# Optimization experiments

Measured on AMD Instinct MI355X. Metric: run time of the kernel, lower is better.

Reference implementation:

```python
import jax, jax.numpy as jnp
import numpy as np

N_NODES = 10000
N_EDGES = 320000
N_PAIRS = 1000000
IN_C = 256
HID_C = 256
LAT_C = 128


def _linear_init(key, fan_in, fan_out, bias=True):
    k1, k2 = jax.random.split(key)
    bound = 1.0 / np.sqrt(fan_in)
    W = jax.random.uniform(k1, (fan_in, fan_out), minval=-bound, maxval=bound, dtype=jnp.float32)
    if bias:
        b = jax.random.uniform(k2, (fan_out,), minval=-bound, maxval=bound, dtype=jnp.float32)
        return W, b
    return W


def setup_inputs() -> dict:
    key = jax.random.key(0)
    ks = jax.random.split(key, 12)
    x = jax.random.normal(ks[0], (N_NODES, IN_C), dtype=jnp.float32)
    edge_index = jax.random.randint(ks[1], (2, N_EDGES), 0, N_NODES, dtype=jnp.int32)
    edge_weight_norm = jax.random.uniform(ks[2], (N_EDGES,), dtype=jnp.float32)
    edge_list = jax.random.randint(ks[3], (2, N_PAIRS), 0, N_NODES, dtype=jnp.int32)
    # GraphConv layer params: lin_rel (bias) on aggregated msgs, lin_root (no bias) on self
    W_rel1, b_rel1 = _linear_init(ks[4], IN_C, HID_C)
    W_root1 = _linear_init(ks[5], IN_C, HID_C, bias=False)
    W_rel2, b_rel2 = _linear_init(ks[6], HID_C, LAT_C)
    W_root2 = _linear_init(ks[7], HID_C, LAT_C, bias=False)
    W_rel3, b_rel3 = _linear_init(ks[8], LAT_C, LAT_C)
    W_root3 = _linear_init(ks[9], LAT_C, LAT_C, bias=False)
    # decoder MLP: Linear(2*LAT, HID) -> ReLU -> Linear(HID, 1)
    Wd1, bd1 = _linear_init(ks[10], 2 * LAT_C, HID_C)
    Wd2, bd2 = _linear_init(ks[11], HID_C, 1)
    return {
        'x': x, 'edge_index': edge_index, 'edge_weight_norm': edge_weight_norm,
        'edge_list': edge_list,
        'W_rel1': W_rel1, 'b_rel1': b_rel1, 'W_root1': W_root1,
        'W_rel2': W_rel2, 'b_rel2': b_rel2, 'W_root2': W_root2,
        'W_rel3': W_rel3, 'b_rel3': b_rel3, 'W_root3': W_root3,
        'Wd1': Wd1, 'bd1': bd1, 'Wd2': Wd2, 'bd2': bd2,
    }


def _graph_conv(h, src, dst, ew, W_rel, b_rel, W_root):
    # message: edge-weighted source features, sum-aggregated at destination
    msg = ew[:, None] * h[src]                        # [E, C_in]
    agg = jax.ops.segment_sum(msg, dst, num_segments=N_NODES)  # [N, C_in]
    return agg @ W_rel + b_rel + h @ W_root           # [N, C_out]


def reference(x, edge_index, edge_weight_norm, edge_list,
              W_rel1, b_rel1, W_root1,
              W_rel2, b_rel2, W_root2,
              W_rel3, b_rel3, W_root3,
              Wd1, bd1, Wd2, bd2):
    src, dst = edge_index[0], edge_index[1]
    h = jax.nn.relu(_graph_conv(x, src, dst, edge_weight_norm, W_rel1, b_rel1, W_root1))
    h = jax.nn.relu(_graph_conv(h, src, dst, edge_weight_norm, W_rel2, b_rel2, W_root2))
    z = _graph_conv(h, src, dst, edge_weight_norm, W_rel3, b_rel3, W_root3)  # [N, LAT]
    # decode edge list: gather pairs, concat, MLP
    h_cat = jnp.concatenate([z[edge_list[0]], z[edge_list[1]]], axis=1)  # [P, 2*LAT]
    hid = jax.nn.relu(h_cat @ Wd1 + bd1)
    out = (hid @ Wd2 + bd2).squeeze(-1)               # [P]
    return out
```

## Files before the change

kernel.cpp:

```cpp
#include <hip/hip_runtime.h>

#define N_NODES 10000
#define N_EDGES 320000
#define N_PAIRS 1000000
#define NBUCK 8
#define DBW 1250
#define SBW 1250
#define PSB 512
#define SLOTB 84
#define GXM 157

typedef unsigned short ushort_t;
typedef __attribute__((ext_vector_type(8))) short short8;
typedef __attribute__((ext_vector_type(4))) float floatx4;
typedef _Float16 half2_t __attribute__((ext_vector_type(2)));

__device__ inline float blo(unsigned int u) { return __uint_as_float(u << 16); }
__device__ inline float bhi(unsigned int u) { return __uint_as_float(u & 0xffff0000u); }
__device__ inline ushort_t f2bf(float f) {
    unsigned int u = __float_as_uint(f);
    unsigned int r = (u + 0x7fffu + ((u >> 16) & 1u)) >> 16;
    return (ushort_t)r;
}
__device__ inline float bf2f(ushort_t b) { return __uint_as_float(((unsigned int)b) << 16); }
__device__ inline void stout(float* p, float v) { *p = v; }
__device__ inline void stout(ushort_t* p, float v) { *p = f2bf(v); }
__device__ inline void stout(_Float16* p, float v) { *p = (_Float16)v; }


__device__ void dev_pstage(int bid, const int* __restrict__ el,
                           int2* __restrict__ stage, int* __restrict__ scnt) {
    __shared__ int lcur[64];
    int t = threadIdx.x;
    if (t < 64) lcur[t] = 0;
    __syncthreads();
    const int STR = PSB * 256;
    int i0 = bid * 256 + t;
#pragma unroll
    for (int k = 0; k < 8; k++) {
        int i = i0 + k * STR;
        if (i < N_PAIRS) {
            int s = el[i], d = el[N_PAIRS + i];
            int c = (d / DBW) * 8 + s / SBW;
            int r = atomicAdd(&lcur[c], 1);
            stage[((size_t)c * PSB + bid) * SLOTB + r] = make_int2(s | (d << 14), i);
        }
    }
    __syncthreads();
    if (t < 64) {
        int n = lcur[t];
        scnt[t * PSB + bid] = n;
        int np = (n + 7) & ~7;
        int2* sp = stage + ((size_t)t * PSB + bid) * SLOTB;
        for (int i = n; i < np; ++i) sp[i] = make_int2(-1, -1);
    }
}

__device__ void dev_hist(int bid, const int* __restrict__ ei, int* __restrict__ cnt) {
    int e = bid * 256 + threadIdx.x;
    if (e < N_EDGES) atomicAdd(&cnt[ei[N_EDGES + e]], 1);
}

__device__ void dev_xsplit(int bid, const float* __restrict__ x, ushort_t* __restrict__ xh) {
    int i = bid * 256 + threadIdx.x;
    if (i >= N_NODES * 256 / 4) return;
    float4 f = ((const float4*)x)[i];
    union { uint2 v; ushort_t u[4]; } H;
    H.u[0] = f2bf(f.x); H.u[1] = f2bf(f.y); H.u[2] = f2bf(f.z); H.u[3] = f2bf(f.w);
    ((uint2*)xh)[i] = H.v;
}

__device__ void dev_wsplit(int bx, int by, int bz,
                           const float* Wr1, const float* Wo1, const float* Wr2, const float* Wo2,
                           const float* Wr3, const float* Wo3, const float* Wd1,
                           ushort_t* r1h, ushort_t* o1h, ushort_t* r2h, ushort_t* o2h,
                           ushort_t* r3h, ushort_t* o3h, ushort_t* dah, ushort_t* dbh) {
    const float* src; ushort_t* dh; int K, NC;
    switch (bz) {
        case 0: src = Wr1; dh = r1h; K = 256; NC = 256; break;
        case 1: src = Wo1; dh = o1h; K = 256; NC = 256; break;
        case 2: src = Wr2; dh = r2h; K = 256; NC = 128; break;
        case 3: src = Wo2; dh = o2h; K = 256; NC = 128; break;
        case 4: src = Wr3; dh = r3h; K = 128; NC = 128; break;
        case 5: src = Wo3; dh = o3h; K = 128; NC = 128; break;
        case 6: src = Wd1;             dh = dah; K = 128; NC = 256; break;
        default: src = Wd1 + 128 * 256; dh = dbh; K = 128; NC = 256; break;
    }
    int tk = bx * 32, tn = by * 32;
    if (tk >= K || tn >= NC) return;
    __shared__ float tile[32][33];
    int tx = threadIdx.x & 31, ty0 = threadIdx.x >> 5;
#pragma unroll
    for (int r = 0; r < 4; r++) {
        int k = tk + ty0 + r * 8;
        tile[ty0 + r * 8][tx] = src[(size_t)k * NC + tn + tx];
    }
    __syncthreads();
#pragma unroll
    for (int r = 0; r < 4; r++) {
        int n = tn + ty0 + r * 8;
        dh[(size_t)n * K + tk + tx] = f2bf(tile[tx][ty0 + r * 8]);
    }
}

__device__ void dev_ealloc(int bid, const int* __restrict__ cnt,
                           int* __restrict__ base_, int* __restrict__ end_,
                           int* __restrict__ cur_, int* __restrict__ tot) {
    __shared__ int part[256];
    __shared__ int bbase;
    int t = threadIdx.x;
    int r = bid * 256 + t;
    int len = (r < N_NODES) ? cnt[r] : 0;
    part[t] = len;
    __syncthreads();
    for (int d = 1; d < 256; d <<= 1) {
        int v = (t >= d) ? part[t - d] : 0;
        __syncthreads();
        part[t] += v;
        __syncthreads();
    }
    if (t == 255) bbase = atomicAdd(tot, part[255]);
    __syncthreads();
    int excl = (t == 0) ? 0 : part[t - 1];
    if (r < N_NODES) {
        int b = bbase + excl;
        base_[r] = b;
        cur_[r] = b;
        end_[r] = b + len;
    }
}

__device__ void dev_scatter(int bid, const int* __restrict__ ei, const float* __restrict__ ew,
                            int* __restrict__ ecur, int2* __restrict__ csr) {
    int e = bid * 256 + threadIdx.x;
    if (e < N_EDGES) {
        int d = ei[N_EDGES + e];
        int pos = atomicAdd(&ecur[d], 1);
        csr[pos] = make_int2(ei[e], __float_as_int(ew[e]));
    }
}

template <bool ALO, typename T1, typename T2>
__device__ void dev_gemm(int bx, int by,
                         const ushort_t* __restrict__ Ahi, const ushort_t* __restrict__ Alo,
                         const ushort_t* __restrict__ W1hi, const ushort_t* __restrict__ W2hi,
                         const float* __restrict__ bias1,
                         T1* __restrict__ out1, T2* __restrict__ out2,
                         int M, int K, int NC) {
    __shared__ ushort_t sAh[64][32], sAl[ALO ? 64 : 1][32];
    __shared__ ushort_t s1h[64][32], s2h[64][32];

    int tid = threadIdx.x;
    int lane = tid & 63, wid = tid >> 6;
    int wm = wid >> 1, wn = wid & 1;
    int l15 = lane & 15, quad = lane >> 4;
    int row0 = bx * 64, col0 = by * 64;

    int srow = tid >> 2, schunk = (tid & 3) * 8;
    int arow = row0 + srow; if (arow > M - 1) arow = M - 1;
    const ushort_t* gAh = Ahi + (size_t)arow * K + schunk;
    const ushort_t* gAl = Alo + (size_t)arow * K + schunk;
    int wrow = col0 + srow;
    const ushort_t* g1h = W1hi + (size_t)wrow * K + schunk;
    const ushort_t* g2h = W2hi + (size_t)wrow * K + schunk;

    floatx4 acc1[2][2] = {}, acc2[2][2] = {};

    for (int kk = 0; kk < K; kk += 32) {
        *(short8*)&sAh[srow][schunk] = *(const short8*)(gAh + kk);
        if (ALO) *(short8*)&sAl[srow][schunk] = *(const short8*)(gAl + kk);
        *(short8*)&s1h[srow][schunk] = *(const short8*)(g1h + kk);
        *(short8*)&s2h[srow][schunk] = *(const short8*)(g2h + kk);
        __syncthreads();

        short8 ah[2], al[2], b1h[2], b2h[2];
#pragma unroll
        for (int t = 0; t < 2; t++) {
            int ar = wm * 32 + t * 16 + l15;
            ah[t] = *(const short8*)&sAh[ar][quad * 8];
            if (ALO) al[t] = *(const short8*)&sAl[ar][quad * 8];
            int bc = wn * 32 + t * 16 + l15;
            b1h[t] = *(const short8*)&s1h[bc][quad * 8];
            b2h[t] = *(const short8*)&s2h[bc][quad * 8];
        }
#pragma unroll
        for (int tm = 0; tm < 2; tm++)
#pragma unroll
            for (int tn = 0; tn < 2; tn++) {
                acc1[tm][tn] = __builtin_amdgcn_mfma_f32_16x16x32_bf16(ah[tm], b1h[tn], acc1[tm][tn], 0, 0, 0);
                acc2[tm][tn] = __builtin_amdgcn_mfma_f32_16x16x32_bf16(ah[tm], b2h[tn], acc2[tm][tn], 0, 0, 0);
                if (ALO) {
                    acc1[tm][tn] = __builtin_amdgcn_mfma_f32_16x16x32_bf16(al[tm], b1h[tn], acc1[tm][tn], 0, 0, 0);
                    acc2[tm][tn] = __builtin_amdgcn_mfma_f32_16x16x32_bf16(al[tm], b2h[tn], acc2[tm][tn], 0, 0, 0);
                }
            }
        __syncthreads();
    }

#pragma unroll
    for (int tm = 0; tm < 2; tm++) {
#pragma unroll
        for (int tn = 0; tn < 2; tn++) {
            int gc = col0 + wn * 32 + tn * 16 + l15;
            float bv = bias1 ? bias1[gc] : 0.f;
#pragma unroll
            for (int reg = 0; reg < 4; reg++) {
                int gr = row0 + wm * 32 + tm * 16 + quad * 4 + reg;
                if (gr >= M) continue;
                stout(&out1[(size_t)gr * NC + gc], acc1[tm][tn][reg] + bv);
                stout(&out2[(size_t)gr * NC + gc], acc2[tm][tn][reg]);
            }
        }
    }
}


__global__ __launch_bounds__(256) void k_fuse1(
    const int* __restrict__ el, int2* __restrict__ stage, int* __restrict__ scnt,
    const int* __restrict__ ei, int* __restrict__ cnt,
    const float* __restrict__ x, ushort_t* __restrict__ ash,
    const float* Wr1, const float* Wo1, const float* Wr2, const float* Wo2,
    const float* Wr3, const float* Wo3, const float* Wd1,
    ushort_t* r1h, ushort_t* o1h, ushort_t* r2h, ushort_t* o2h,
    ushort_t* r3h, ushort_t* o3h, ushort_t* dah, ushort_t* dbh) {
    int b = blockIdx.x;
    if (b < PSB) { dev_pstage(b, el, stage, scnt); return; }
    b -= PSB;
    if (b < 1250) { dev_hist(b, ei, cnt); return; }
    b -= 1250;
    if (b < 2500) { dev_xsplit(b, x, ash); return; }
    b -= 2500;
    dev_wsplit(b & 7, (b >> 3) & 7, b >> 6, Wr1, Wo1, Wr2, Wo2, Wr3, Wo3, Wd1,
               r1h, o1h, r2h, o2h, r3h, o3h, dah, dbh);
}

__global__ __launch_bounds__(256) void k_ealloc(const int* __restrict__ cnt,
                                                int* __restrict__ ebase, int* __restrict__ eend,
                                                int* __restrict__ ecur, int* __restrict__ etot) {
    dev_ealloc(blockIdx.x, cnt, ebase, eend, ecur, etot);
}

__global__ __launch_bounds__(256) void k_fuse3(
    const int* __restrict__ ei, const float* __restrict__ ew, int* __restrict__ ecur,
    int2* __restrict__ csr,
    const ushort_t* __restrict__ ash, const ushort_t* __restrict__ asl,
    const ushort_t* __restrict__ r1h, const ushort_t* __restrict__ o1h,
    ushort_t* __restrict__ Pb, float* __restrict__ Rb) {
    int b = blockIdx.x;
    if (b < 1250) { dev_scatter(b, ei, ew, ecur, csr); return; }
    b -= 1250;
    dev_gemm<false, ushort_t, float>(b % GXM, b / GXM, ash, asl, r1h, o1h, nullptr,
                                     Pb, Rb, N_NODES, 256, 256);
}

template <bool ALO, typename T1, typename T2>
__global__ __launch_bounds__(256) void k_gemm_bf(const ushort_t* __restrict__ Ahi, const ushort_t* __restrict__ Alo,
                                                 const ushort_t* __restrict__ W1hi, const ushort_t* __restrict__ W2hi,
                                                 const float* __restrict__ bias1,
                                                 T1* __restrict__ out1, T2* __restrict__ out2,
                                                 int M, int K, int NC) {
    dev_gemm<ALO, T1, T2>(blockIdx.x, blockIdx.y, Ahi, Alo, W1hi, W2hi, bias1, out1, out2, M, K, NC);
}

template <int C, bool RELU, bool EMITLO>
__global__ __launch_bounds__(256) void k_aggf(const ushort_t* __restrict__ P, const float* __restrict__ R,
                                              const float* __restrict__ bias,
                                              const int* __restrict__ ebase, const int* __restrict__ eend,
                                              const int2* __restrict__ csr,
                                              ushort_t* __restrict__ hh, ushort_t* __restrict__ hl) {
    int wave = (blockIdx.x * 256 + threadIdx.x) >> 6;
    int lane = threadIdx.x & 63;
    if (wave >= N_NODES) return;
    int beg = ebase[wave], end = eend[wave];
    if constexpr (C == 256) {
        int col = lane * 4;
        float4 acc = {0.f, 0.f, 0.f, 0.f};
        int e = beg;
        int2 p0, p1, p2, p3;
        if (e + 3 < end) { p0 = csr[e]; p1 = csr[e + 1]; p2 = csr[e + 2]; p3 = csr[e + 3]; }
        for (; e + 3 < end; ) {
            float w0 = __int_as_float(p0.y), w1 = __int_as_float(p1.y);
            float w2 = __int_as_float(p2.y), w3 = __int_as_float(p3.y);
            uint2 u0 = *(const uint2*)&P[(size_t)p0.x * 256 + col];
            uint2 u1 = *(const uint2*)&P[(size_t)p1.x * 256 + col];
            uint2 u2 = *(const uint2*)&P[(size_t)p2.x * 256 + col];
            uint2 u3 = *(const uint2*)&P[(size_t)p3.x * 256 + col];
            int en = e + 4;
            if (en + 3 < end) { p0 = csr[en]; p1 = csr[en + 1]; p2 = csr[en + 2]; p3 = csr[en + 3]; }
            acc.x += w0 * blo(u0.x) + w1 * blo(u1.x);
            acc.y += w0 * bhi(u0.x) + w1 * bhi(u1.x);
            acc.z += w0 * blo(u0.y) + w1 * blo(u1.y);
            acc.w += w0 * bhi(u0.y) + w1 * bhi(u1.y);
            acc.x += w2 * blo(u2.x) + w3 * blo(u3.x);
            acc.y += w2 * bhi(u2.x) + w3 * bhi(u3.x);
            acc.z += w2 * blo(u2.y) + w3 * blo(u3.y);
            acc.w += w2 * bhi(u2.y) + w3 * bhi(u3.y);
            e = en;
        }
        for (; e + 1 < end; e += 2) {
            int2 q0 = csr[e], q1 = csr[e + 1];
            float w0 = __int_as_float(q0.y), w1 = __int_as_float(q1.y);
            uint2 u0 = *(const uint2*)&P[(size_t)q0.x * 256 + col];
            uint2 u1 = *(const uint2*)&P[(size_t)q1.x * 256 + col];
            acc.x += w0 * blo(u0.x) + w1 * blo(u1.x);
            acc.y += w0 * bhi(u0.x) + w1 * bhi(u1.x);
            acc.z += w0 * blo(u0.y) + w1 * blo(u1.y);
            acc.w += w0 * bhi(u0.y) + w1 * bhi(u1.y);
        }
        if (e < end) {
            int2 q0 = csr[e];
            float w0 = __int_as_float(q0.y);
            uint2 u0 = *(const uint2*)&P[(size_t)q0.x * 256 + col];
            acc.x += w0 * blo(u0.x); acc.y += w0 * bhi(u0.x);
            acc.z += w0 * blo(u0.y); acc.w += w0 * bhi(u0.y);
        }
        float4 rr = *(const float4*)&R[(size_t)wave * 256 + col];
        float4 bb = *(const float4*)&bias[col];
        float o[4];
        o[0] = acc.x + rr.x + bb.x; o[1] = acc.y + rr.y + bb.y;
        o[2] = acc.z + rr.z + bb.z; o[3] = acc.w + rr.w + bb.w;
        if (RELU) {
#pragma unroll
            for (int j = 0; j < 4; j++) o[j] = fmaxf(o[j], 0.f);
        }
        union { uint2 v; ushort_t u[4]; } H, L;
#pragma unroll
        for (int j = 0; j < 4; j++) {
            ushort_t h = f2bf(o[j]);
            H.u[j] = h;
            if (EMITLO) L.u[j] = f2bf(o[j] - bf2f(h));
        }
        *(uint2*)&hh[(size_t)wave * 256 + col] = H.v;
        if (EMITLO) *(uint2*)&hl[(size_t)wave * 256 + col] = L.v;
    } else {
        int col = lane * 2;
        float2 acc = {0.f, 0.f};
        int e = beg;
        int2 p0, p1, p2, p3;
        if (e + 3 < end) { p0 = csr[e]; p1 = csr[e + 1]; p2 = csr[e + 2]; p3 = csr[e + 3]; }
        for (; e + 3 < end; ) {
            float w0 = __int_as_float(p0.y), w1 = __int_as_float(p1.y);
            float w2 = __int_as_float(p2.y), w3 = __int_as_float(p3.y);
            unsigned int u0 = *(const unsigned int*)&P[(size_t)p0.x * 128 + col];
            unsigned int u1 = *(const unsigned int*)&P[(size_t)p1.x * 128 + col];
            unsigned int u2 = *(const unsigned int*)&P[(size_t)p2.x * 128 + col];
            unsigned int u3 = *(const unsigned int*)&P[(size_t)p3.x * 128 + col];
            int en = e + 4;
            if (en + 3 < end) { p0 = csr[en]; p1 = csr[en + 1]; p2 = csr[en + 2]; p3 = csr[en + 3]; }
            acc.x += w0 * blo(u0) + w1 * blo(u1);
            acc.y += w0 * bhi(u0) + w1 * bhi(u1);
            acc.x += w2 * blo(u2) + w3 * blo(u3);
            acc.y += w2 * bhi(u2) + w3 * bhi(u3);
            e = en;
        }
        for (; e + 1 < end; e += 2) {
            int2 q0 = csr[e], q1 = csr[e + 1];
            float w0 = __int_as_float(q0.y), w1 = __int_as_float(q1.y);
            unsigned int u0 = *(const unsigned int*)&P[(size_t)q0.x * 128 + col];
            unsigned int u1 = *(const unsigned int*)&P[(size_t)q1.x * 128 + col];
            acc.x += w0 * blo(u0) + w1 * blo(u1);
            acc.y += w0 * bhi(u0) + w1 * bhi(u1);
        }
        if (e < end) {
            int2 q0 = csr[e];
            float w0 = __int_as_float(q0.y);
            unsigned int u0 = *(const unsigned int*)&P[(size_t)q0.x * 128 + col];
            acc.x += w0 * blo(u0); acc.y += w0 * bhi(u0);
        }
        float2 rr = *(const float2*)&R[(size_t)wave * 128 + col];
        float2 bb = *(const float2*)&bias[col];
        float o0 = acc.x + rr.x + bb.x, o1 = acc.y + rr.y + bb.y;
        if (RELU) { o0 = fmaxf(o0, 0.f); o1 = fmaxf(o1, 0.f); }
        union { unsigned int v; ushort_t u[2]; } H, L;
        ushort_t h0 = f2bf(o0), h1 = f2bf(o1);
        H.u[0] = h0; H.u[1] = h1;
        *(unsigned int*)&hh[(size_t)wave * 128 + col] = H.v;
        if (EMITLO) {
            L.u[0] = f2bf(o0 - bf2f(h0)); L.u[1] = f2bf(o1 - bf2f(h1));
            *(unsigned int*)&hl[(size_t)wave * 128 + col] = L.v;
        }
    }
}

__device__ inline float dot8relu_f16(uint4 ua, uint4 ub, const half2_t* w2p) {
    half2_t z = {(_Float16)0.f, (_Float16)0.f};
    float r = 0.f;
    half2_t s;
    s = __builtin_elementwise_max(__builtin_bit_cast(half2_t, ua.x) + __builtin_bit_cast(half2_t, ub.x), z);
    r = __builtin_amdgcn_fdot2(s, w2p[0], r, false);
    s = __builtin_elementwise_max(__builtin_bit_cast(half2_t, ua.y) + __builtin_bit_cast(half2_t, ub.y), z);
    r = __builtin_amdgcn_fdot2(s, w2p[1], r, false);
    s = __builtin_elementwise_max(__builtin_bit_cast(half2_t, ua.z) + __builtin_bit_cast(half2_t, ub.z), z);
    r = __builtin_amdgcn_fdot2(s, w2p[2], r, false);
    s = __builtin_elementwise_max(__builtin_bit_cast(half2_t, ua.w) + __builtin_bit_cast(half2_t, ub.w), z);
    r = __builtin_amdgcn_fdot2(s, w2p[3], r, false);
    return r;
}

__global__ __launch_bounds__(256) void k_decoder(const _Float16* __restrict__ Ab, const _Float16* __restrict__ Bb,
                                                 const int2* __restrict__ stage, const int* __restrict__ scnt,
                                                 const float* __restrict__ Wd2, const float* __restrict__ bd2,
                                                 float* __restrict__ out) {
    int x = blockIdx.x & 7;
    int t = blockIdx.x >> 3;
    int sb = t >> 6;
    int bi = t & 63;
    int hw = threadIdx.x >> 5;
    int l32 = threadIdx.x & 31;
    int pb = bi * 8 + hw;
    int c = x * 8 + sb;
    int n = scnt[c * PSB + pb];
    int ng = (n + 7) >> 3;
    const int2* sp = stage + ((size_t)c * PSB + pb) * SLOTB;
    int col = l32 * 8;
    half2_t w2p[4];
#pragma unroll
    for (int q = 0; q < 4; q++) {
        half2_t w = {(_Float16)Wd2[col + 2 * q], (_Float16)Wd2[col + 2 * q + 1]};
        w2p[q] = w;
    }
    float b2 = bd2[0];
    const char* Ac = (const char*)Ab + (size_t)col * 2;
    const char* Bc = (const char*)Bb + (size_t)col * 2;

    for (int g = 0; g < ng; ++g) {
        int4 q0 = *(const int4*)&sp[g * 8];
        int4 q1 = *(const int4*)&sp[g * 8 + 2];
        int4 q2 = *(const int4*)&sp[g * 8 + 4];
        int4 q3 = *(const int4*)&sp[g * 8 + 6];
        int w0 = max(q0.x, 0), w1 = max(q0.z, 0);
        int w2i = max(q1.x, 0), w3 = max(q1.z, 0);
        int w4 = max(q2.x, 0), w5 = max(q2.z, 0);
        int w6 = max(q3.x, 0), w7 = max(q3.z, 0);
        uint4 a0 = *(const uint4*)(Ac + ((w0 & 16383) << 9));
        uint4 b0 = *(const uint4*)(Bc + ((w0 >> 14) << 9));
        uint4 a1 = *(const uint4*)(Ac + ((w1 & 16383) << 9));
        uint4 b1 = *(const uint4*)(Bc + ((w1 >> 14) << 9));
        uint4 a2 = *(const uint4*)(Ac + ((w2i & 16383) << 9));
        uint4 b2v = *(const uint4*)(Bc + ((w2i >> 14) << 9));
        uint4 a3 = *(const uint4*)(Ac + ((w3 & 16383) << 9));
        uint4 b3 = *(const uint4*)(Bc + ((w3 >> 14) << 9));
        uint4 a4 = *(const uint4*)(Ac + ((w4 & 16383) << 9));
        uint4 b4 = *(const uint4*)(Bc + ((w4 >> 14) << 9));
        uint4 a5 = *(const uint4*)(Ac + ((w5 & 16383) << 9));
        uint4 b5 = *(const uint4*)(Bc + ((w5 >> 14) << 9));
        uint4 a6 = *(const uint4*)(Ac + ((w6 & 16383) << 9));
        uint4 b6 = *(const uint4*)(Bc + ((w6 >> 14) << 9));
        uint4 a7 = *(const uint4*)(Ac + ((w7 & 16383) << 9));
        uint4 b7 = *(const uint4*)(Bc + ((w7 >> 14) << 9));
        float r0 = dot8relu_f16(a0, b0, w2p);
        float r1 = dot8relu_f16(a1, b1, w2p);
        float r2 = dot8relu_f16(a2, b2v, w2p);
        float r3 = dot8relu_f16(a3, b3, w2p);
        float r4 = dot8relu_f16(a4, b4, w2p);
        float r5 = dot8relu_f16(a5, b5, w2p);
        float r6 = dot8relu_f16(a6, b6, w2p);
        float r7 = dot8relu_f16(a7, b7, w2p);
        float u01 = (l32 & 1) ? r1 : r0, v01 = (l32 & 1) ? r0 : r1;
        u01 += __shfl_xor(v01, 1, 32);
        float u23 = (l32 & 1) ? r3 : r2, v23 = (l32 & 1) ? r2 : r3;
        u23 += __shfl_xor(v23, 1, 32);
        float u45 = (l32 & 1) ? r5 : r4, v45 = (l32 & 1) ? r4 : r5;
        u45 += __shfl_xor(v45, 1, 32);
        float u67 = (l32 & 1) ? r7 : r6, v67 = (l32 & 1) ? r6 : r7;
        u67 += __shfl_xor(v67, 1, 32);
        float w03 = (l32 & 2) ? u23 : u01, wv03 = (l32 & 2) ? u01 : u23;
        w03 += __shfl_xor(wv03, 2, 32);
        float w47 = (l32 & 2) ? u67 : u45, wv47 = (l32 & 2) ? u45 : u67;
        w47 += __shfl_xor(wv47, 2, 32);
        float v = (l32 & 4) ? w47 : w03, vv = (l32 & 4) ? w03 : w47;
        v += __shfl_xor(vv, 4, 32);
        v += __shfl_xor(v, 8, 32);
        v += __shfl_xor(v, 16, 32);
        int pA = (l32 & 1) ? q0.w : q0.y;
        int pB = (l32 & 1) ? q1.w : q1.y;
        int pC = (l32 & 1) ? q2.w : q2.y;
        int pD = (l32 & 1) ? q3.w : q3.y;
        int pAB = (l32 & 2) ? pB : pA;
        int pCD = (l32 & 2) ? pD : pC;
        int p = (l32 & 4) ? pCD : pAB;
        if (l32 < 8 && p >= 0) out[p] = v + b2;
    }
}

extern "C" void kernel_launch(void* const* d_in, const int* in_sizes, int n_in,
                              void* d_out, int out_size, void* d_ws, size_t ws_size,
                              hipStream_t stream) {
    const float* x   = (const float*)d_in[0];
    const int*   ei  = (const int*)d_in[1];
    const float* ew  = (const float*)d_in[2];
    const int*   el  = (const int*)d_in[3];
    const float* Wr1 = (const float*)d_in[4];
    const float* br1 = (const float*)d_in[5];
    const float* Wo1 = (const float*)d_in[6];
    const float* Wr2 = (const float*)d_in[7];
    const float* br2 = (const float*)d_in[8];
    const float* Wo2 = (const float*)d_in[9];
    const float* Wr3 = (const float*)d_in[10];
    const float* br3 = (const float*)d_in[11];
    const float* Wo3 = (const float*)d_in[12];
    const float* Wd1 = (const float*)d_in[13];
    const float* bd1 = (const float*)d_in[14];
    const float* Wd2 = (const float*)d_in[15];
    const float* bd2 = (const float*)d_in[16];
    float* out = (float*)d_out;

    char* ws = (char*)d_ws;
    size_t o = 0;
    auto alloc = [&](size_t bytes) { size_t p = o; o += (bytes + 255) & ~(size_t)255; return (void*)(ws + p); };
    int*     cnt     = (int*)alloc(N_NODES * 4);
    int*     etot    = (int*)alloc(4);
    size_t   zero_bytes = (size_t)((char*)etot - (char*)cnt) + 256;
    int2*    stage   = (int2*)alloc((size_t)64 * PSB * SLOTB * 8);
    int*     scnt    = (int*)alloc((size_t)64 * PSB * 4);
    int2*    csr     = (int2*)alloc((size_t)N_EDGES * 8);
    int*     ebase   = (int*)alloc(N_NODES * 4);
    int*     eend    = (int*)alloc(N_NODES * 4);
    int*     ecur    = (int*)alloc(N_NODES * 4);
    ushort_t* ash = (ushort_t*)alloc((size_t)N_NODES * 256 * 2);
    ushort_t* asl = (ushort_t*)alloc((size_t)N_NODES * 256 * 2);
    ushort_t* Pb  = (ushort_t*)alloc((size_t)N_NODES * 256 * 2);
    float*    Rb  = (float*)alloc((size_t)N_NODES * 256 * 4);
    ushort_t* r1h = (ushort_t*)alloc(256 * 256 * 2);
    ushort_t* o1h = (ushort_t*)alloc(256 * 256 * 2);
    ushort_t* r2h = (ushort_t*)alloc(128 * 256 * 2);
    ushort_t* o2h = (ushort_t*)alloc(128 * 256 * 2);
    ushort_t* r3h = (ushort_t*)alloc(128 * 128 * 2);
    ushort_t* o3h = (ushort_t*)alloc(128 * 128 * 2);
    ushort_t* dah = (ushort_t*)alloc(256 * 128 * 2);
    ushort_t* dbh = (ushort_t*)alloc(256 * 128 * 2);
    _Float16* Atab = (_Float16*)Pb;
    _Float16* Btab = (_Float16*)Rb;

    hipMemsetAsync(cnt, 0, zero_bytes, stream);

    k_fuse1<<<4774, 256, 0, stream>>>(el, stage, scnt, ei, cnt, x, ash,
                                      Wr1, Wo1, Wr2, Wo2, Wr3, Wo3, Wd1,
                                      r1h, o1h, r2h, o2h, r3h, o3h, dah, dbh);
    k_ealloc<<<40, 256, 0, stream>>>(cnt, ebase, eend, ecur, etot);
    k_fuse3<<<1878, 256, 0, stream>>>(ei, ew, ecur, csr, ash, asl, r1h, o1h, Pb, Rb);

    k_aggf<256, true, false><<<2500, 256, 0, stream>>>(Pb, Rb, br1, ebase, eend, csr, ash, asl);

    k_gemm_bf<false, ushort_t, float><<<dim3(GXM, 2), 256, 0, stream>>>(ash, asl, r2h, o2h, nullptr,
                                                                        Pb, Rb, N_NODES, 256, 128);
    k_aggf<128, true, false><<<2500, 256, 0, stream>>>(Pb, Rb, br2, ebase, eend, csr, ash, asl);

    k_gemm_bf<false, ushort_t, float><<<dim3(GXM, 2), 256, 0, stream>>>(ash, asl, r3h, o3h, nullptr,
                                                                        Pb, Rb, N_NODES, 128, 128);
    k_aggf<128, false, true><<<2500, 256, 0, stream>>>(Pb, Rb, br3, ebase, eend, csr, ash, asl);

    k_gemm_bf<true, _Float16, _Float16><<<dim3(GXM, 4), 256, 0, stream>>>(ash, asl, dah, dbh, bd1,
                                                                          Atab, Btab, N_NODES, 128, 256);

    k_decoder<<<4096, 256, 0, stream>>>(Atab, Btab, stage, scnt, Wd2, bd2, out);
}
```

Measured before the change: 295.1 us.

## Replace CSR prefix-scan build with fixed-capacity per-node edge slots

Builds the destination-grouped edge list by scattering each edge straight into a fixed 84-slot region per node, using an atomic per-node counter. This happens inside the first fused kernel, so the histogram, the prefix-scan allocation kernel and the separate scatter pass all go away. The layer-1 GEMM now runs as its own launch instead of being fused with the scatter. The aggregation kernels get each node's range from node*SLOTE and the count. This removes a kernel launch and a dependent pass over the edges, at the cost of a larger sparse edge buffer and an assumption that no node exceeds 84 in-edges.

```diff
diff --git a/kernel.cpp b/kernel.cpp
--- a/kernel.cpp
+++ b/kernel.cpp
@@ -8,6 +8,7 @@
 #define SBW 1250
 #define PSB 512
 #define SLOTB 84
+#define SLOTE 84
 #define GXM 157
 
 typedef unsigned short ushort_t;
@@ -56,9 +57,14 @@
     }
 }
 
-__device__ void dev_hist(int bid, const int* __restrict__ ei, int* __restrict__ cnt) {
+__device__ void dev_scatter(int bid, const int* __restrict__ ei, const float* __restrict__ ew,
+                            int* __restrict__ ecnt, int2* __restrict__ csr) {
     int e = bid * 256 + threadIdx.x;
-    if (e < N_EDGES) atomicAdd(&cnt[ei[N_EDGES + e]], 1);
+    if (e < N_EDGES) {
+        int d = ei[N_EDGES + e];
+        int r = atomicAdd(&ecnt[d], 1);
+        csr[(size_t)d * SLOTE + r] = make_int2(ei[e], __float_as_int(ew[e]));
+    }
 }
 
 __device__ void dev_xsplit(int bid, const float* __restrict__ x, ushort_t* __restrict__ xh) {
@@ -103,43 +109,6 @@
     }
 }
 
-__device__ void dev_ealloc(int bid, const int* __restrict__ cnt,
-                           int* __restrict__ base_, int* __restrict__ end_,
-                           int* __restrict__ cur_, int* __restrict__ tot) {
-    __shared__ int part[256];
-    __shared__ int bbase;
-    int t = threadIdx.x;
-    int r = bid * 256 + t;
-    int len = (r < N_NODES) ? cnt[r] : 0;
-    part[t] = len;
-    __syncthreads();
-    for (int d = 1; d < 256; d <<= 1) {
-        int v = (t >= d) ? part[t - d] : 0;
-        __syncthreads();
-        part[t] += v;
-        __syncthreads();
-    }
-    if (t == 255) bbase = atomicAdd(tot, part[255]);
-    __syncthreads();
-    int excl = (t == 0) ? 0 : part[t - 1];
-    if (r < N_NODES) {
-        int b = bbase + excl;
-        base_[r] = b;
-        cur_[r] = b;
-        end_[r] = b + len;
-    }
-}
-
-__device__ void dev_scatter(int bid, const int* __restrict__ ei, const float* __restrict__ ew,
-                            int* __restrict__ ecur, int2* __restrict__ csr) {
-    int e = bid * 256 + threadIdx.x;
-    if (e < N_EDGES) {
-        int d = ei[N_EDGES + e];
-        int pos = atomicAdd(&ecur[d], 1);
-        csr[pos] = make_int2(ei[e], __float_as_int(ew[e]));
-    }
-}
-
 template <bool ALO, typename T1, typename T2>
 __device__ void dev_gemm(int bx, int by,
                          const ushort_t* __restrict__ Ahi, const ushort_t* __restrict__ Alo,
@@ -217,7 +186,8 @@
 
 __global__ __launch_bounds__(256) void k_fuse1(
     const int* __restrict__ el, int2* __restrict__ stage, int* __restrict__ scnt,
-    const int* __restrict__ ei, int* __restrict__ cnt,
+    const int* __restrict__ ei, const float* __restrict__ ew,
+    int* __restrict__ ecnt, int2* __restrict__ csr,
     const float* __restrict__ x, ushort_t* __restrict__ ash,
     const float* Wr1, const float* Wo1, const float* Wr2, const float* Wo2,
     const float* Wr3, const float* Wo3, const float* Wd1,
@@ -226,31 +196,12 @@
     int b = blockIdx.x;
     if (b < PSB) { dev_pstage(b, el, stage, scnt); return; }
     b -= PSB;
-    if (b < 1250) { dev_hist(b, ei, cnt); return; }
+    if (b < 1250) { dev_scatter(b, ei, ew, ecnt, csr); return; }
     b -= 1250;
     if (b < 2500) { dev_xsplit(b, x, ash); return; }
     b -= 2500;
     dev_wsplit(b & 7, (b >> 3) & 7, b >> 6, Wr1, Wo1, Wr2, Wo2, Wr3, Wo3, Wd1,
                r1h, o1h, r2h, o2h, r3h, o3h, dah, dbh);
-}
-
-__global__ __launch_bounds__(256) void k_ealloc(const int* __restrict__ cnt,
-                                                int* __restrict__ ebase, int* __restrict__ eend,
-                                                int* __restrict__ ecur, int* __restrict__ etot) {
-    dev_ealloc(blockIdx.x, cnt, ebase, eend, ecur, etot);
-}
-
-__global__ __launch_bounds__(256) void k_fuse3(
-    const int* __restrict__ ei, const float* __restrict__ ew, int* __restrict__ ecur,
-    int2* __restrict__ csr,
-    const ushort_t* __restrict__ ash, const ushort_t* __restrict__ asl,
-    const ushort_t* __restrict__ r1h, const ushort_t* __restrict__ o1h,
-    ushort_t* __restrict__ Pb, float* __restrict__ Rb) {
-    int b = blockIdx.x;
-    if (b < 1250) { dev_scatter(b, ei, ew, ecur, csr); return; }
-    b -= 1250;
-    dev_gemm<false, ushort_t, float>(b % GXM, b / GXM, ash, asl, r1h, o1h, nullptr,
-                                     Pb, Rb, N_NODES, 256, 256);
 }
 
 template <bool ALO, typename T1, typename T2>
@@ -265,13 +216,13 @@
 template <int C, bool RELU, bool EMITLO>
 __global__ __launch_bounds__(256) void k_aggf(const ushort_t* __restrict__ P, const float* __restrict__ R,
                                               const float* __restrict__ bias,
-                                              const int* __restrict__ ebase, const int* __restrict__ eend,
+                                              const int* __restrict__ ecnt,
                                               const int2* __restrict__ csr,
                                               ushort_t* __restrict__ hh, ushort_t* __restrict__ hl) {
     int wave = (blockIdx.x * 256 + threadIdx.x) >> 6;
     int lane = threadIdx.x & 63;
     if (wave >= N_NODES) return;
-    int beg = ebase[wave], end = eend[wave];
+    int beg = wave * SLOTE, end = beg + ecnt[wave];
     if constexpr (C == 256) {
         int col = lane * 4;
         float4 acc = {0.f, 0.f, 0.f, 0.f};
@@ -508,15 +459,10 @@
     char* ws = (char*)d_ws;
     size_t o = 0;
     auto alloc = [&](size_t bytes) { size_t p = o; o += (bytes + 255) & ~(size_t)255; return (void*)(ws + p); };
-    int*     cnt     = (int*)alloc(N_NODES * 4);
-    int*     etot    = (int*)alloc(4);
-    size_t   zero_bytes = (size_t)((char*)etot - (char*)cnt) + 256;
+    int*     ecnt    = (int*)alloc(N_NODES * 4);
     int2*    stage   = (int2*)alloc((size_t)64 * PSB * SLOTB * 8);
     int*     scnt    = (int*)alloc((size_t)64 * PSB * 4);
-    int2*    csr     = (int2*)alloc((size_t)N_EDGES * 8);
-    int*     ebase   = (int*)alloc(N_NODES * 4);
-    int*     eend    = (int*)alloc(N_NODES * 4);
-    int*     ecur    = (int*)alloc(N_NODES * 4);
+    int2*    csr     = (int2*)alloc((size_t)N_NODES * SLOTE * 8);
     ushort_t* ash = (ushort_t*)alloc((size_t)N_NODES * 256 * 2);
     ushort_t* asl = (ushort_t*)alloc((size_t)N_NODES * 256 * 2);
     ushort_t* Pb  = (ushort_t*)alloc((size_t)N_NODES * 256 * 2);
@@ -532,23 +478,23 @@
     _Float16* Atab = (_Float16*)Pb;
     _Float16* Btab = (_Float16*)Rb;
 
-    hipMemsetAsync(cnt, 0, zero_bytes, stream);
-
-    k_fuse1<<<4774, 256, 0, stream>>>(el, stage, scnt, ei, cnt, x, ash,
+    hipMemsetAsync(ecnt, 0, N_NODES * 4, stream);
+
+    k_fuse1<<<4774, 256, 0, stream>>>(el, stage, scnt, ei, ew, ecnt, csr, x, ash,
                                       Wr1, Wo1, Wr2, Wo2, Wr3, Wo3, Wd1,
                                       r1h, o1h, r2h, o2h, r3h, o3h, dah, dbh);
-    k_ealloc<<<40, 256, 0, stream>>>(cnt, ebase, eend, ecur, etot);
-    k_fuse3<<<1878, 256, 0, stream>>>(ei, ew, ecur, csr, ash, asl, r1h, o1h, Pb, Rb);
-
-    k_aggf<256, true, false><<<2500, 256, 0, stream>>>(Pb, Rb, br1, ebase, eend, csr, ash, asl);
+
+    k_gemm_bf<false, ushort_t, float><<<dim3(GXM, 4), 256, 0, stream>>>(ash, asl, r1h, o1h, nullptr,
+                                                                        Pb, Rb, N_NODES, 256, 256);
+    k_aggf<256, true, false><<<2500, 256, 0, stream>>>(Pb, Rb, br1, ecnt, csr, ash, asl);
 
     k_gemm_bf<false, ushort_t, float><<<dim3(GXM, 2), 256, 0, stream>>>(ash, asl, r2h, o2h, nullptr,
                                                                         Pb, Rb, N_NODES, 256, 128);
-    k_aggf<128, true, false><<<2500, 256, 0, stream>>>(Pb, Rb, br2, ebase, eend, csr, ash, asl);
+    k_aggf<128, true, false><<<2500, 256, 0, stream>>>(Pb, Rb, br2, ecnt, csr, ash, asl);
 
     k_gemm_bf<false, ushort_t, float><<<dim3(GXM, 2), 256, 0, stream>>>(ash, asl, r3h, o3h, nullptr,
                                                                         Pb, Rb, N_NODES, 128, 128);
-    k_aggf<128, false, true><<<2500, 256, 0, stream>>>(Pb, Rb, br3, ebase, eend, csr, ash, asl);
+    k_aggf<128, false, true><<<2500, 256, 0, stream>>>(Pb, Rb, br3, ecnt, csr, ash, asl);
 
     k_gemm_bf<true, _Float16, _Float16><<<dim3(GXM, 4), 256, 0, stream>>>(ash, asl, dah, dbh, bd1,
                                                                           Atab, Btab, N_NODES, 128, 256);
```

After: 273.7 us. 1.08x faster.
